# Kernel tuning notes

Hardware: AMD Instinct MI355X
Metric: run time of the kernel (lower is better)

## Reference

```python
import jax, jax.numpy as jnp
import numpy as np

T, B, E, H = 512, 32, 512, 2048

def setup_inputs() -> dict:
    key = jax.random.key(0)
    k1, k2, k3 = jax.random.split(key, 3)
    sent = jax.random.normal(k1, (T, B, E), dtype=jnp.float32)
    lengths = jax.random.randint(k2, (B,), 1, T + 1)  # unused by the math (pack is never applied)
    # Linear(E, 3H) params (PyTorch default-ish init scale)
    W = jax.random.normal(k3, (3 * H, E), dtype=jnp.float32) * (1.0 / np.sqrt(E))
    b = jnp.zeros((3 * H,), dtype=jnp.float32)
    return {"sent": sent, "lengths": lengths, "W": W, "b": b}

def reference(sent, lengths, W, b):
    # sent: (T, B, E) time-major. Single QRNN layer, window=1, output_gate=True, zoneout=0.
    Y = jnp.einsum('tbe,he->tbh', sent, W) + b          # (T, B, 3H)
    Z, F, O = jnp.split(Y, 3, axis=-1)
    Z = jnp.tanh(Z)
    F = jax.nn.sigmoid(F)
    O = jax.nn.sigmoid(O)

    # forget-mult recurrence: c_t = f_t * z_t + (1 - f_t) * c_{t-1}, c_0 = 0
    def step(c, zf):
        z, f = zf
        c = f * z + (1.0 - f) * c
        return c, c
    c0 = jnp.zeros_like(Z[0])                            # (B, H)
    _, C = jax.lax.scan(step, c0, (Z, F))                # (T, B, H)

    Hseq = O * C                                         # QRNN output (T, B, H)
    embeds = jnp.max(Hseq, axis=0)                       # torch.max(sent_output, 0)[0] -> (B, H)
    return embeds
```

## Files before the change

### kernel.cpp

```cpp
#include <hip/hip_runtime.h>
#include <stdint.h>

#define TT 512
#define BB 32
#define EE 512
#define HH 2048

typedef __attribute__((ext_vector_type(8))) short short8;
typedef __attribute__((ext_vector_type(4))) float f32x4;

#define XROW 528
#define XBUF (16 * XROW)

static __device__ __forceinline__ unsigned short f2bf(float f) {
    union { float f; unsigned u; } v; v.f = f;
    unsigned u = v.u;
    unsigned r = u + 0x7FFFu + ((u >> 16) & 1u);
    return (unsigned short)(r >> 16);
}

static __device__ __forceinline__ float fast_exp(float x) {
    return __builtin_amdgcn_exp2f(x * 1.44269504f);
}
static __device__ __forceinline__ float fast_rcp(float x) {
    return __builtin_amdgcn_rcpf(x);
}

static __device__ __forceinline__ void load_lds16(const unsigned short* g, unsigned short* l) {
    __builtin_amdgcn_global_load_lds(
        (const __attribute__((address_space(1))) unsigned int*)(uintptr_t)g,
        (__attribute__((address_space(3))) unsigned int*)(uintptr_t)l,
        16, 0, 0);
}

__global__ void convert_inputs(const float* __restrict__ X,
                               const float* __restrict__ W,
                               unsigned short* __restrict__ Xb,
                               unsigned short* __restrict__ Wb) {
    const int nX = TT * BB * EE;
    int i = (blockIdx.x * blockDim.x + threadIdx.x) * 8;
    const float* src;
    unsigned short* dst;
    int j;
    if (i < nX) { src = X; dst = Xb; j = i; }
    else        { src = W; dst = Wb; j = i - nX; }
    float4 v0 = *(const float4*)(src + j);
    float4 v1 = *(const float4*)(src + j + 4);
    union { short8 s; unsigned short u[8]; } o;
    o.u[0] = f2bf(v0.x); o.u[1] = f2bf(v0.y); o.u[2] = f2bf(v0.z); o.u[3] = f2bf(v0.w);
    o.u[4] = f2bf(v1.x); o.u[5] = f2bf(v1.y); o.u[6] = f2bf(v1.z); o.u[7] = f2bf(v1.w);
    *(short8*)(dst + j) = o.s;
}

__launch_bounds__(256, 2)
__global__ void qrnn_fused(const unsigned short* __restrict__ Xb,
                           const unsigned short* __restrict__ Wb,
                           const float* __restrict__ bias,
                           float* __restrict__ out)
{
    __shared__ unsigned short xlds[2 * XBUF];
    __shared__ float exch[2][2][64][12];

    const int tid  = threadIdx.x;
    const int wv   = tid >> 6;
    const int lane = tid & 63;
    const int q    = lane >> 4;
    const int c    = lane & 15;
    const int hi   = wv >> 1;
    const int s    = wv & 1;
    const int b    = blockIdx.y;
    const int h    = blockIdx.x * 32 + hi * 16 + c;

    short8 wz[8], wf[8], wo[8];
    {
        const unsigned short* wzr = Wb + (size_t)h * EE            + s * 256;
        const unsigned short* wfr = Wb + (size_t)(HH + h) * EE     + s * 256;
        const unsigned short* wor = Wb + (size_t)(2 * HH + h) * EE + s * 256;
#pragma unroll
        for (int k = 0; k < 8; ++k) {
            int e0 = k * 32 + q * 8;
            wz[k] = *(const short8*)(wzr + e0);
            wf[k] = *(const short8*)(wfr + e0);
            wo[k] = *(const short8*)(wor + e0);
        }
    }
#pragma unroll
    for (int k = 0; k < 8; ++k) {
        asm volatile("" : "+a"(wz[k]), "+a"(wf[k]), "+a"(wo[k]));
    }

    const float b0 = (s == 0) ? bias[h]          : 0.0f;
    const float b1 = (s == 0) ? bias[HH + h]     : 0.0f;
    const float b2 = (s == 0) ? bias[2 * HH + h] : 0.0f;

    float carry = 0.0f;
    float vmax  = -1e30f;

    const unsigned short* g0 = Xb + ((size_t)(wv * 4) * BB + b) * EE + lane * 8;
    unsigned short* l0 = &xlds[(wv * 4) * XROW];

    auto stage = [&](int n, int slot) {
        const unsigned short* g = g0 + (size_t)n * (16 * BB * EE);
        unsigned short* l = l0 + slot * XBUF;
#pragma unroll
        for (int i = 0; i < 4; ++i)
            load_lds16(g + (size_t)i * (BB * EE), l + i * XROW);
    };

    stage(0, 0);
    __syncthreads();

    for (int ch = 0; ch < 32; ++ch) {
        const int buf = ch & 1;
        if (ch < 31) stage(ch + 1, buf ^ 1);

        const unsigned short* Abase = &xlds[buf * XBUF + c * XROW + s * 256 + q * 8];
        short8 a[8];
#pragma unroll
        for (int k = 0; k < 8; ++k)
            a[k] = *(const short8*)(Abase + k * 32);

        f32x4 az = {b0, b0, b0, b0};
        f32x4 af = {b1, b1, b1, b1};
        f32x4 ao = {b2, b2, b2, b2};
#pragma unroll
        for (int k = 0; k < 8; ++k) {
            az = __builtin_amdgcn_mfma_f32_16x16x32_bf16(a[k], wz[k], az, 0, 0, 0);
            af = __builtin_amdgcn_mfma_f32_16x16x32_bf16(a[k], wf[k], af, 0, 0, 0);
            ao = __builtin_amdgcn_mfma_f32_16x16x32_bf16(a[k], wo[k], ao, 0, 0, 0);
        }

        const int eb = ch & 1;
        if (s == 1) {
            float* e = &exch[eb][hi][lane][0];
            *(f32x4*)(e)     = az;
            *(f32x4*)(e + 4) = af;
            *(f32x4*)(e + 8) = ao;
        }

        __syncthreads();

        if (s == 0) {
            const float* e = &exch[eb][hi][lane][0];
            f32x4 pz = *(const f32x4*)(e);
            f32x4 pf = *(const f32x4*)(e + 4);
            f32x4 po = *(const f32x4*)(e + 8);
            az = az + pz; af = af + pf; ao = ao + po;

            float aa[4], mm[4], oo[4];
#pragma unroll
            for (int r = 0; r < 4; ++r) {
                float e2 = fast_exp(2.0f * az[r]);
                float z  = 1.0f - 2.0f * fast_rcp(e2 + 1.0f);
                float f  = fast_rcp(1.0f + fast_exp(-af[r]));
                float o  = fast_rcp(1.0f + fast_exp(-ao[r]));
                aa[r] = f * z;
                mm[r] = 1.0f - f;
                oo[r] = o;
            }

            float A = aa[0], M = mm[0];
#pragma unroll
            for (int r = 1; r < 4; ++r) { A = aa[r] + mm[r] * A; M = mm[r] * M; }

            float Ap = __shfl_up(A, 16, 64), Mp = __shfl_up(M, 16, 64);
            if (q >= 1) { A = A + M * Ap; M = M * Mp; }
            Ap = __shfl_up(A, 32, 64); Mp = __shfl_up(M, 32, 64);
            if (q >= 2) { A = A + M * Ap; M = M * Mp; }
            float Ae = __shfl_up(A, 16, 64), Me = __shfl_up(M, 16, 64);
            if (q == 0) { Ae = 0.0f; Me = 1.0f; }
            float cc = Ae + Me * carry;

#pragma unroll
            for (int r = 0; r < 4; ++r) {
                cc = aa[r] + mm[r] * cc;
                vmax = fmaxf(vmax, oo[r] * cc);
            }

            float cend = A + M * carry;
            carry = __shfl(cend, 48 + c, 64);
        }
    }

    if (s == 0) {
        vmax = fmaxf(vmax, __shfl_xor(vmax, 16, 64));
        vmax = fmaxf(vmax, __shfl_xor(vmax, 32, 64));
        if (q == 0) out[(size_t)b * HH + h] = vmax;
    }
}

extern "C" void kernel_launch(void* const* d_in, const int* in_sizes, int n_in,
                              void* d_out, int out_size, void* d_ws, size_t ws_size,
                              hipStream_t stream) {
    const float* sent = (const float*)d_in[0];
    const float* W    = (const float*)d_in[2];
    const float* bias = (const float*)d_in[3];
    float* out        = (float*)d_out;

    const int nX = TT * BB * EE;
    const int nW = 3 * HH * EE;
    unsigned short* Xb = (unsigned short*)d_ws;
    unsigned short* Wb = Xb + nX;

    int totalVec = (nX + nW) / 8;
    convert_inputs<<<totalVec / 256, 256, 0, stream>>>(sent, W, Xb, Wb);

    dim3 grid(HH / 32, BB);
    qrnn_fused<<<grid, 256, 0, stream>>>(Xb, Wb, bias, out);
}
```

Before: 215.5 us.

## Software-pipeline the scan one chunk behind the MFMA and convert W in-kernel

The fused kernel now runs the nonlinearity and scan for chunk ch-1 while the MFMAs for chunk ch are issued, so the serial scan overlaps with tensor-core work and there is one barrier per iteration. The weights are now read as fp32 and converted to bf16 inside the fused kernel, so the separate conversion of W to a workspace is dropped. The in-kernel conversion uses scalar fp32 loads and each W row is re-converted by all 32 batch blocks, so it adds redundant global reads at kernel start. The pipelining also keeps extra accumulator registers live across iterations.

```diff
diff --git a/kernel.cpp b/kernel.cpp
--- a/kernel.cpp
+++ b/kernel.cpp
@@ -34,27 +34,19 @@
 }
 
 __global__ void convert_inputs(const float* __restrict__ X,
-                               const float* __restrict__ W,
-                               unsigned short* __restrict__ Xb,
-                               unsigned short* __restrict__ Wb) {
-    const int nX = TT * BB * EE;
+                               unsigned short* __restrict__ Xb) {
     int i = (blockIdx.x * blockDim.x + threadIdx.x) * 8;
-    const float* src;
-    unsigned short* dst;
-    int j;
-    if (i < nX) { src = X; dst = Xb; j = i; }
-    else        { src = W; dst = Wb; j = i - nX; }
-    float4 v0 = *(const float4*)(src + j);
-    float4 v1 = *(const float4*)(src + j + 4);
+    float4 v0 = *(const float4*)(X + i);
+    float4 v1 = *(const float4*)(X + i + 4);
     union { short8 s; unsigned short u[8]; } o;
     o.u[0] = f2bf(v0.x); o.u[1] = f2bf(v0.y); o.u[2] = f2bf(v0.z); o.u[3] = f2bf(v0.w);
     o.u[4] = f2bf(v1.x); o.u[5] = f2bf(v1.y); o.u[6] = f2bf(v1.z); o.u[7] = f2bf(v1.w);
-    *(short8*)(dst + j) = o.s;
+    *(short8*)(Xb + i) = o.s;
 }
 
 __launch_bounds__(256, 2)
 __global__ void qrnn_fused(const unsigned short* __restrict__ Xb,
-                           const unsigned short* __restrict__ Wb,
+                           const float* __restrict__ Wf,
                            const float* __restrict__ bias,
                            float* __restrict__ out)
 {
@@ -73,15 +65,20 @@
 
     short8 wz[8], wf[8], wo[8];
     {
-        const unsigned short* wzr = Wb + (size_t)h * EE            + s * 256;
-        const unsigned short* wfr = Wb + (size_t)(HH + h) * EE     + s * 256;
-        const unsigned short* wor = Wb + (size_t)(2 * HH + h) * EE + s * 256;
+        const float* wzr = Wf + (size_t)h * EE            + s * 256;
+        const float* wfr = Wf + (size_t)(HH + h) * EE     + s * 256;
+        const float* wor = Wf + (size_t)(2 * HH + h) * EE + s * 256;
 #pragma unroll
         for (int k = 0; k < 8; ++k) {
             int e0 = k * 32 + q * 8;
-            wz[k] = *(const short8*)(wzr + e0);
-            wf[k] = *(const short8*)(wfr + e0);
-            wo[k] = *(const short8*)(wor + e0);
+            union { short8 s8; unsigned short u[8]; } pz, pf, po;
+#pragma unroll
+            for (int j = 0; j < 8; ++j) {
+                pz.u[j] = f2bf(wzr[e0 + j]);
+                pf.u[j] = f2bf(wfr[e0 + j]);
+                po.u[j] = f2bf(wor[e0 + j]);
+            }
+            wz[k] = pz.s8; wf[k] = pf.s8; wo[k] = po.s8;
         }
     }
 #pragma unroll
@@ -110,50 +107,46 @@
     stage(0, 0);
     __syncthreads();
 
-    for (int ch = 0; ch < 32; ++ch) {
+    f32x4 yz = {0,0,0,0}, yf = {0,0,0,0}, yo = {0,0,0,0};
+
+    for (int ch = 0; ch <= 32; ++ch) {
         const int buf = ch & 1;
         if (ch < 31) stage(ch + 1, buf ^ 1);
 
-        const unsigned short* Abase = &xlds[buf * XBUF + c * XROW + s * 256 + q * 8];
-        short8 a[8];
-#pragma unroll
-        for (int k = 0; k < 8; ++k)
-            a[k] = *(const short8*)(Abase + k * 32);
-
-        f32x4 az = {b0, b0, b0, b0};
-        f32x4 af = {b1, b1, b1, b1};
-        f32x4 ao = {b2, b2, b2, b2};
-#pragma unroll
-        for (int k = 0; k < 8; ++k) {
-            az = __builtin_amdgcn_mfma_f32_16x16x32_bf16(a[k], wz[k], az, 0, 0, 0);
-            af = __builtin_amdgcn_mfma_f32_16x16x32_bf16(a[k], wf[k], af, 0, 0, 0);
-            ao = __builtin_amdgcn_mfma_f32_16x16x32_bf16(a[k], wo[k], ao, 0, 0, 0);
-        }
-
-        const int eb = ch & 1;
-        if (s == 1) {
-            float* e = &exch[eb][hi][lane][0];
-            *(f32x4*)(e)     = az;
-            *(f32x4*)(e + 4) = af;
-            *(f32x4*)(e + 8) = ao;
-        }
-
-        __syncthreads();
-
-        if (s == 0) {
+        f32x4 az, af, ao;
+        if (ch < 32) {
+            const unsigned short* Abase = &xlds[buf * XBUF + c * XROW + s * 256 + q * 8];
+            short8 a[8];
+#pragma unroll
+            for (int k = 0; k < 8; ++k)
+                a[k] = *(const short8*)(Abase + k * 32);
+
+            az = (f32x4){b0, b0, b0, b0};
+            af = (f32x4){b1, b1, b1, b1};
+            ao = (f32x4){b2, b2, b2, b2};
+#pragma unroll
+            for (int k = 0; k < 8; ++k) {
+                az = __builtin_amdgcn_mfma_f32_16x16x32_bf16(a[k], wz[k], az, 0, 0, 0);
+                af = __builtin_amdgcn_mfma_f32_16x16x32_bf16(a[k], wf[k], af, 0, 0, 0);
+                ao = __builtin_amdgcn_mfma_f32_16x16x32_bf16(a[k], wo[k], ao, 0, 0, 0);
+            }
+        }
+
+        if (ch > 0 && s == 0) {
+            const int eb = (ch - 1) & 1;
             const float* e = &exch[eb][hi][lane][0];
             f32x4 pz = *(const f32x4*)(e);
             f32x4 pf = *(const f32x4*)(e + 4);
             f32x4 po = *(const f32x4*)(e + 8);
-            az = az + pz; af = af + pf; ao = ao + po;
+            f32x4 tz = yz + pz, tf = yf + pf, to = yo + po;
 
             float aa[4], mm[4], oo[4];
 #pragma unroll
             for (int r = 0; r < 4; ++r) {
-                float e2 = fast_exp(2.0f * az[r]);
+                float e2 = fast_exp(2.0f * tz[r]);
                 float z  = 1.0f - 2.0f * fast_rcp(e2 + 1.0f);
-                float f  = fast_rcp(1.0f + fast_exp(-af[r]));
-                float o  = fast_rcp(1.0f + fast_exp(-ao[r]));
+                float f  = fast_rcp(1.0f + fast_exp(-tf[r]));
+                float o  = fast_rcp(1.0f + fast_exp(-to[r]));
                 aa[r] = f * z;
                 mm[r] = 1.0f - f;
                 oo[r] = o;
@@ -180,6 +173,17 @@
             float cend = A + M * carry;
             carry = __shfl(cend, 48 + c, 64);
         }
+
+        if (ch < 32 && s == 1) {
+            float* e = &exch[buf][hi][lane][0];
+            *(f32x4*)(e)     = az;
+            *(f32x4*)(e + 4) = af;
+            *(f32x4*)(e + 8) = ao;
+        }
+
+        if (ch < 32) __syncthreads();
+
+        if (ch < 32 && s == 0) { yz = az; yf = af; yo = ao; }
     }
 
     if (s == 0) {
@@ -198,13 +202,10 @@
     float* out        = (float*)d_out;
 
     const int nX = TT * BB * EE;
-    const int nW = 3 * HH * EE;
     unsigned short* Xb = (unsigned short*)d_ws;
-    unsigned short* Wb = Xb + nX;
-
-    int totalVec = (nX + nW) / 8;
-    convert_inputs<<<totalVec / 256, 256, 0, stream>>>(sent, W, Xb, Wb);
+
+    convert_inputs<<<nX / 8 / 256, 256, 0, stream>>>(sent, Xb);
 
     dim3 grid(HH / 32, BB);
-    qrnn_fused<<<grid, 256, 0, stream>>>(Xb, Wb, bias, out);
-}
+    qrnn_fused<<<grid, 256, 0, stream>>>(Xb, W, bias, out);
+}
```

New measurement: 252.8 us. 1.17x slower.

## Process 32 timesteps per chunk with single-buffered LDS and interleaved MFMA streams

Applied to the files above, without the earlier changes.

Doubles the timestep chunk from 16 to 32 and drops the LDS double buffer. Operands are loaded into registers first, then a barrier lets the next chunk's global-to-LDS staging overlap the MFMAs. The two 16-step sub-tiles run as interleaved independent MFMA chains and a two-segment scan, which halves the chunk iterations and barriers. The cost is more registers and an extra barrier per chunk, and with one buffer a chunk's prefetch can no longer start until every wave has finished reading the previous one.

```diff
diff --git a/kernel.cpp b/kernel.cpp
--- a/kernel.cpp
+++ b/kernel.cpp
@@ -10,7 +10,7 @@
 typedef __attribute__((ext_vector_type(4))) float f32x4;
 
 #define XROW 528
-#define XBUF (16 * XROW)
+#define XBUF (32 * XROW)
 
 static __device__ __forceinline__ unsigned short f2bf(float f) {
     union { float f; unsigned u; } v; v.f = f;
@@ -18,14 +18,12 @@
     unsigned r = u + 0x7FFFu + ((u >> 16) & 1u);
     return (unsigned short)(r >> 16);
 }
-
 static __device__ __forceinline__ float fast_exp(float x) {
     return __builtin_amdgcn_exp2f(x * 1.44269504f);
 }
 static __device__ __forceinline__ float fast_rcp(float x) {
     return __builtin_amdgcn_rcpf(x);
 }
-
 static __device__ __forceinline__ void load_lds16(const unsigned short* g, unsigned short* l) {
     __builtin_amdgcn_global_load_lds(
         (const __attribute__((address_space(1))) unsigned int*)(uintptr_t)g,
@@ -58,8 +56,8 @@
                            const float* __restrict__ bias,
                            float* __restrict__ out)
 {
-    __shared__ unsigned short xlds[2 * XBUF];
-    __shared__ float exch[2][2][64][12];
+    __shared__ unsigned short xlds[XBUF];
+    __shared__ float exch[2][64][28];
 
     const int tid  = threadIdx.x;
     const int wv   = tid >> 6;
@@ -96,89 +94,109 @@
     float carry = 0.0f;
     float vmax  = -1e30f;
 
-    const unsigned short* g0 = Xb + ((size_t)(wv * 4) * BB + b) * EE + lane * 8;
-    unsigned short* l0 = &xlds[(wv * 4) * XROW];
-
-    auto stage = [&](int n, int slot) {
-        const unsigned short* g = g0 + (size_t)n * (16 * BB * EE);
-        unsigned short* l = l0 + slot * XBUF;
-#pragma unroll
-        for (int i = 0; i < 4; ++i)
-            load_lds16(g + (size_t)i * (BB * EE), l + i * XROW);
+    const unsigned short* g0 = Xb + ((size_t)(wv * 8) * BB + b) * EE + lane * 8;
+    unsigned short* l0 = &xlds[(wv * 8) * XROW];
+    auto stage = [&](int n) {
+        const unsigned short* g = g0 + (size_t)n * (32 * BB * EE);
+#pragma unroll
+        for (int i = 0; i < 8; ++i)
+            load_lds16(g + (size_t)i * (BB * EE), l0 + i * XROW);
     };
 
-    stage(0, 0);
+    stage(0);
     __syncthreads();
 
-    for (int ch = 0; ch < 32; ++ch) {
-        const int buf = ch & 1;
-        if (ch < 31) stage(ch + 1, buf ^ 1);
-
-        const unsigned short* Abase = &xlds[buf * XBUF + c * XROW + s * 256 + q * 8];
-        short8 a[8];
-#pragma unroll
-        for (int k = 0; k < 8; ++k)
-            a[k] = *(const short8*)(Abase + k * 32);
-
-        f32x4 az = {b0, b0, b0, b0};
-        f32x4 af = {b1, b1, b1, b1};
-        f32x4 ao = {b2, b2, b2, b2};
+#pragma unroll 1
+    for (int ch = 0; ch < 16; ++ch) {
+        const unsigned short* Ab = &xlds[c * XROW + s * 256 + q * 8];
+        short8 a0[8], a1[8];
 #pragma unroll
         for (int k = 0; k < 8; ++k) {
-            az = __builtin_amdgcn_mfma_f32_16x16x32_bf16(a[k], wz[k], az, 0, 0, 0);
-            af = __builtin_amdgcn_mfma_f32_16x16x32_bf16(a[k], wf[k], af, 0, 0, 0);
-            ao = __builtin_amdgcn_mfma_f32_16x16x32_bf16(a[k], wo[k], ao, 0, 0, 0);
-        }
-
-        const int eb = ch & 1;
+            a0[k] = *(const short8*)(Ab + k * 32);
+            a1[k] = *(const short8*)(Ab + 16 * XROW + k * 32);
+        }
+
+        __syncthreads();
+
+        if (ch < 15) stage(ch + 1);
+
+        f32x4 az0 = {b0,b0,b0,b0}, af0 = {b1,b1,b1,b1}, ao0 = {b2,b2,b2,b2};
+        f32x4 az1 = {b0,b0,b0,b0}, af1 = {b1,b1,b1,b1}, ao1 = {b2,b2,b2,b2};
+#pragma unroll
+        for (int k = 0; k < 8; ++k) {
+            az0 = __builtin_amdgcn_mfma_f32_16x16x32_bf16(a0[k], wz[k], az0, 0, 0, 0);
+            az1 = __builtin_amdgcn_mfma_f32_16x16x32_bf16(a1[k], wz[k], az1, 0, 0, 0);
+            af0 = __builtin_amdgcn_mfma_f32_16x16x32_bf16(a0[k], wf[k], af0, 0, 0, 0);
+            af1 = __builtin_amdgcn_mfma_f32_16x16x32_bf16(a1[k], wf[k], af1, 0, 0, 0);
+            ao0 = __builtin_amdgcn_mfma_f32_16x16x32_bf16(a0[k], wo[k], ao0, 0, 0, 0);
+            ao1 = __builtin_amdgcn_mfma_f32_16x16x32_bf16(a1[k], wo[k], ao1, 0, 0, 0);
+        }
+
         if (s == 1) {
-            float* e = &exch[eb][hi][lane][0];
-            *(f32x4*)(e)     = az;
-            *(f32x4*)(e + 4) = af;
-            *(f32x4*)(e + 8) = ao;
+            float* e = &exch[hi][lane][0];
+            *(f32x4*)(e +  0) = az0;  *(f32x4*)(e +  4) = af0;  *(f32x4*)(e +  8) = ao0;
+            *(f32x4*)(e + 12) = az1;  *(f32x4*)(e + 16) = af1;  *(f32x4*)(e + 20) = ao1;
         }
 
         __syncthreads();
 
         if (s == 0) {
-            const float* e = &exch[eb][hi][lane][0];
-            f32x4 pz = *(const f32x4*)(e);
-            f32x4 pf = *(const f32x4*)(e + 4);
-            f32x4 po = *(const f32x4*)(e + 8);
-            az = az + pz; af = af + pf; ao = ao + po;
-
-            float aa[4], mm[4], oo[4];
+            const float* e = &exch[hi][lane][0];
+            f32x4 tz0 = az0 + *(const f32x4*)(e +  0);
+            f32x4 tf0 = af0 + *(const f32x4*)(e +  4);
+            f32x4 to0 = ao0 + *(const f32x4*)(e +  8);
+            f32x4 tz1 = az1 + *(const f32x4*)(e + 12);
+            f32x4 tf1 = af1 + *(const f32x4*)(e + 16);
+            f32x4 to1 = ao1 + *(const f32x4*)(e + 20);
+
+            float aa[2][4], mm[2][4], oo[2][4];
 #pragma unroll
             for (int r = 0; r < 4; ++r) {
-                float e2 = fast_exp(2.0f * az[r]);
+                float e2 = fast_exp(2.0f * tz0[r]);
                 float z  = 1.0f - 2.0f * fast_rcp(e2 + 1.0f);
-                float f  = fast_rcp(1.0f + fast_exp(-af[r]));
-                float o  = fast_rcp(1.0f + fast_exp(-ao[r]));
-                aa[r] = f * z;
-                mm[r] = 1.0f - f;
-                oo[r] = o;
-            }
-
-            float A = aa[0], M = mm[0];
-#pragma unroll
-            for (int r = 1; r < 4; ++r) { A = aa[r] + mm[r] * A; M = mm[r] * M; }
-
-            float Ap = __shfl_up(A, 16, 64), Mp = __shfl_up(M, 16, 64);
-            if (q >= 1) { A = A + M * Ap; M = M * Mp; }
-            Ap = __shfl_up(A, 32, 64); Mp = __shfl_up(M, 32, 64);
-            if (q >= 2) { A = A + M * Ap; M = M * Mp; }
-            float Ae = __shfl_up(A, 16, 64), Me = __shfl_up(M, 16, 64);
-            if (q == 0) { Ae = 0.0f; Me = 1.0f; }
-            float cc = Ae + Me * carry;
-
+                float f  = fast_rcp(1.0f + fast_exp(-tf0[r]));
+                oo[0][r] = fast_rcp(1.0f + fast_exp(-to0[r]));
+                aa[0][r] = f * z;  mm[0][r] = 1.0f - f;
+                float e2b = fast_exp(2.0f * tz1[r]);
+                float zb  = 1.0f - 2.0f * fast_rcp(e2b + 1.0f);
+                float fb  = fast_rcp(1.0f + fast_exp(-tf1[r]));
+                oo[1][r] = fast_rcp(1.0f + fast_exp(-to1[r]));
+                aa[1][r] = fb * zb;  mm[1][r] = 1.0f - fb;
+            }
+
+            float A0 = aa[0][0], M0 = mm[0][0], A1 = aa[1][0], M1 = mm[1][0];
+#pragma unroll
+            for (int r = 1; r < 4; ++r) {
+                A0 = aa[0][r] + mm[0][r] * A0;  M0 = mm[0][r] * M0;
+                A1 = aa[1][r] + mm[1][r] * A1;  M1 = mm[1][r] * M1;
+            }
+            float Ap, Mp, Bp, Np;
+            Ap = __shfl_up(A0, 16, 64); Mp = __shfl_up(M0, 16, 64);
+            Bp = __shfl_up(A1, 16, 64); Np = __shfl_up(M1, 16, 64);
+            if (q >= 1) { A0 = A0 + M0 * Ap; M0 *= Mp; A1 = A1 + M1 * Bp; M1 *= Np; }
+            Ap = __shfl_up(A0, 32, 64); Mp = __shfl_up(M0, 32, 64);
+            Bp = __shfl_up(A1, 32, 64); Np = __shfl_up(M1, 32, 64);
+            if (q >= 2) { A0 = A0 + M0 * Ap; M0 *= Mp; A1 = A1 + M1 * Bp; M1 *= Np; }
+            float fA0 = __shfl(A0, 48 + c, 64), fM0 = __shfl(M0, 48 + c, 64);
+            float fA1 = __shfl(A1, 48 + c, 64), fM1 = __shfl(M1, 48 + c, 64);
+            float eA0 = __shfl_up(A0, 16, 64), eM0 = __shfl_up(M0, 16, 64);
+            float eA1 = __shfl_up(A1, 16, 64), eM1 = __shfl_up(M1, 16, 64);
+            if (q == 0) { eA0 = 0.0f; eM0 = 1.0f; eA1 = 0.0f; eM1 = 1.0f; }
+
+            float cc = eA0 + eM0 * carry;
 #pragma unroll
             for (int r = 0; r < 4; ++r) {
-                cc = aa[r] + mm[r] * cc;
-                vmax = fmaxf(vmax, oo[r] * cc);
-            }
-
-            float cend = A + M * carry;
-            carry = __shfl(cend, 48 + c, 64);
+                cc = aa[0][r] + mm[0][r] * cc;
+                vmax = fmaxf(vmax, oo[0][r] * cc);
+            }
+            float base1 = fA0 + fM0 * carry;
+            cc = eA1 + eM1 * base1;
+#pragma unroll
+            for (int r = 0; r < 4; ++r) {
+                cc = aa[1][r] + mm[1][r] * cc;
+                vmax = fmaxf(vmax, oo[1][r] * cc);
+            }
+            carry = fA1 + fM1 * base1;
         }
     }
 
```

After: 231.0 us. 1.07x slower.

## Split GEMM and scan into dedicated warps with a one-chunk software pipeline

Applied to the files above, without the earlier changes.

The block grows from 4 to 6 waves. Four waves only run the MFMA GEMM and write partial sums to a double-buffered LDS exchange. Two extra waves add the partials, apply bias and the activations, and run the forget-mult scan one chunk behind. This is meant to overlap the serial scan and transcendental work with the next chunk's matrix multiply instead of running them back to back. In exchange it adds an extra loop iteration, more LDS traffic for the exchange, and more threads per block, which may reduce occupancy under launch bounds of 384 threads with 2 blocks per unit.

```diff
diff --git a/kernel.cpp b/kernel.cpp
--- a/kernel.cpp
+++ b/kernel.cpp
@@ -18,14 +18,12 @@
     unsigned r = u + 0x7FFFu + ((u >> 16) & 1u);
     return (unsigned short)(r >> 16);
 }
-
 static __device__ __forceinline__ float fast_exp(float x) {
     return __builtin_amdgcn_exp2f(x * 1.44269504f);
 }
 static __device__ __forceinline__ float fast_rcp(float x) {
     return __builtin_amdgcn_rcpf(x);
 }
-
 static __device__ __forceinline__ void load_lds16(const unsigned short* g, unsigned short* l) {
     __builtin_amdgcn_global_load_lds(
         (const __attribute__((address_space(1))) unsigned int*)(uintptr_t)g,
@@ -52,27 +50,29 @@
     *(short8*)(dst + j) = o.s;
 }
 
-__launch_bounds__(256, 2)
+__launch_bounds__(384, 2)
 __global__ void qrnn_fused(const unsigned short* __restrict__ Xb,
                            const unsigned short* __restrict__ Wb,
                            const float* __restrict__ bias,
                            float* __restrict__ out)
 {
     __shared__ unsigned short xlds[2 * XBUF];
-    __shared__ float exch[2][2][64][12];
+    __shared__ float exch[2][2][2][64][12];
 
     const int tid  = threadIdx.x;
     const int wv   = tid >> 6;
     const int lane = tid & 63;
     const int q    = lane >> 4;
     const int c    = lane & 15;
-    const int hi   = wv >> 1;
+    const int b    = blockIdx.y;
+    const bool isGemm = (wv < 4);
+    const int hi   = (wv >> 1) & 1;
     const int s    = wv & 1;
-    const int b    = blockIdx.y;
-    const int h    = blockIdx.x * 32 + hi * 16 + c;
+    const int shi  = wv - 4;
 
     short8 wz[8], wf[8], wo[8];
-    {
+    if (isGemm) {
+        const int h = blockIdx.x * 32 + hi * 16 + c;
         const unsigned short* wzr = Wb + (size_t)h * EE            + s * 256;
         const unsigned short* wfr = Wb + (size_t)(HH + h) * EE     + s * 256;
         const unsigned short* wor = Wb + (size_t)(2 * HH + h) * EE + s * 256;
@@ -83,22 +83,25 @@
             wf[k] = *(const short8*)(wfr + e0);
             wo[k] = *(const short8*)(wor + e0);
         }
-    }
-#pragma unroll
-    for (int k = 0; k < 8; ++k) {
-        asm volatile("" : "+a"(wz[k]), "+a"(wf[k]), "+a"(wo[k]));
-    }
-
-    const float b0 = (s == 0) ? bias[h]          : 0.0f;
-    const float b1 = (s == 0) ? bias[HH + h]     : 0.0f;
-    const float b2 = (s == 0) ? bias[2 * HH + h] : 0.0f;
+#pragma unroll
+        for (int k = 0; k < 8; ++k) {
+            asm volatile("" : "+a"(wz[k]), "+a"(wf[k]), "+a"(wo[k]));
+        }
+    }
+
+    float bz = 0.f, bfg = 0.f, bog = 0.f;
+    if (!isGemm) {
+        const int h = blockIdx.x * 32 + shi * 16 + c;
+        bz  = bias[h];
+        bfg = bias[HH + h];
+        bog = bias[2 * HH + h];
+    }
 
     float carry = 0.0f;
     float vmax  = -1e30f;
 
-    const unsigned short* g0 = Xb + ((size_t)(wv * 4) * BB + b) * EE + lane * 8;
-    unsigned short* l0 = &xlds[(wv * 4) * XROW];
-
+    const unsigned short* g0 = Xb + ((size_t)((wv & 3) * 4) * BB + b) * EE + lane * 8;
+    unsigned short* l0 = &xlds[((wv & 3) * 4) * XROW];
     auto stage = [&](int n, int slot) {
         const unsigned short* g = g0 + (size_t)n * (16 * BB * EE);
         unsigned short* l = l0 + slot * XBUF;
@@ -107,53 +110,53 @@
             load_lds16(g + (size_t)i * (BB * EE), l + i * XROW);
     };
 
-    stage(0, 0);
+    if (isGemm) stage(0, 0);
     __syncthreads();
 
-    for (int ch = 0; ch < 32; ++ch) {
-        const int buf = ch & 1;
-        if (ch < 31) stage(ch + 1, buf ^ 1);
-
-        const unsigned short* Abase = &xlds[buf * XBUF + c * XROW + s * 256 + q * 8];
-        short8 a[8];
-#pragma unroll
-        for (int k = 0; k < 8; ++k)
-            a[k] = *(const short8*)(Abase + k * 32);
-
-        f32x4 az = {b0, b0, b0, b0};
-        f32x4 af = {b1, b1, b1, b1};
-        f32x4 ao = {b2, b2, b2, b2};
-#pragma unroll
-        for (int k = 0; k < 8; ++k) {
-            az = __builtin_amdgcn_mfma_f32_16x16x32_bf16(a[k], wz[k], az, 0, 0, 0);
-            af = __builtin_amdgcn_mfma_f32_16x16x32_bf16(a[k], wf[k], af, 0, 0, 0);
-            ao = __builtin_amdgcn_mfma_f32_16x16x32_bf16(a[k], wo[k], ao, 0, 0, 0);
-        }
-
-        const int eb = ch & 1;
-        if (s == 1) {
-            float* e = &exch[eb][hi][lane][0];
-            *(f32x4*)(e)     = az;
-            *(f32x4*)(e + 4) = af;
-            *(f32x4*)(e + 8) = ao;
-        }
-
-        __syncthreads();
-
-        if (s == 0) {
-            const float* e = &exch[eb][hi][lane][0];
-            f32x4 pz = *(const f32x4*)(e);
-            f32x4 pf = *(const f32x4*)(e + 4);
-            f32x4 po = *(const f32x4*)(e + 8);
-            az = az + pz; af = af + pf; ao = ao + po;
+#pragma unroll 1
+    for (int ch = 0; ch <= 32; ++ch) {
+        if (isGemm) {
+            if (ch < 32) {
+                const int buf = ch & 1;
+                if (ch < 31) stage(ch + 1, buf ^ 1);
+
+                const unsigned short* Ab = &xlds[buf * XBUF + c * XROW + s * 256 + q * 8];
+                short8 a[8];
+#pragma unroll
+                for (int k = 0; k < 8; ++k)
+                    a[k] = *(const short8*)(Ab + k * 32);
+
+                f32x4 az = {0.f,0.f,0.f,0.f}, af = {0.f,0.f,0.f,0.f}, ao = {0.f,0.f,0.f,0.f};
+#pragma unroll
+                for (int k = 0; k < 8; ++k) {
+                    az = __builtin_amdgcn_mfma_f32_16x16x32_bf16(a[k], wz[k], az, 0, 0, 0);
+                    af = __builtin_amdgcn_mfma_f32_16x16x32_bf16(a[k], wf[k], af, 0, 0, 0);
+                    ao = __builtin_amdgcn_mfma_f32_16x16x32_bf16(a[k], wo[k], ao, 0, 0, 0);
+                }
+
+                float* e = &exch[buf][hi][s][lane][0];
+                *(f32x4*)(e)     = az;
+                *(f32x4*)(e + 4) = af;
+                *(f32x4*)(e + 8) = ao;
+            }
+        } else if (ch > 0) {
+            const int slot = (ch - 1) & 1;
+            const float* e0 = &exch[slot][shi][0][lane][0];
+            const float* e1 = &exch[slot][shi][1][lane][0];
+            f32x4 tz = *(const f32x4*)(e0)     + *(const f32x4*)(e1);
+            f32x4 tf = *(const f32x4*)(e0 + 4) + *(const f32x4*)(e1 + 4);
+            f32x4 to = *(const f32x4*)(e0 + 8) + *(const f32x4*)(e1 + 8);
 
             float aa[4], mm[4], oo[4];
 #pragma unroll
             for (int r = 0; r < 4; ++r) {
-                float e2 = fast_exp(2.0f * az[r]);
+                float yz = tz[r] + bz;
+                float yf = tf[r] + bfg;
+                float yo = to[r] + bog;
+                float e2 = fast_exp(2.0f * yz);
                 float z  = 1.0f - 2.0f * fast_rcp(e2 + 1.0f);
-                float f  = fast_rcp(1.0f + fast_exp(-af[r]));
-                float o  = fast_rcp(1.0f + fast_exp(-ao[r]));
+                float f  = fast_rcp(1.0f + fast_exp(-yf));
+                float o  = fast_rcp(1.0f + fast_exp(-yo));
                 aa[r] = f * z;
                 mm[r] = 1.0f - f;
                 oo[r] = o;
@@ -180,12 +183,17 @@
             float cend = A + M * carry;
             carry = __shfl(cend, 48 + c, 64);
         }
-    }
-
-    if (s == 0) {
+
+        __syncthreads();
+    }
+
+    if (!isGemm) {
         vmax = fmaxf(vmax, __shfl_xor(vmax, 16, 64));
         vmax = fmaxf(vmax, __shfl_xor(vmax, 32, 64));
-        if (q == 0) out[(size_t)b * HH + h] = vmax;
+        if (q == 0) {
+            const int h = blockIdx.x * 32 + shi * 16 + c;
+            out[(size_t)b * HH + h] = vmax;
+        }
     }
 }
 
@@ -206,5 +214,5 @@
     convert_inputs<<<totalVec / 256, 256, 0, stream>>>(sent, W, Xb, Wb);
 
     dim3 grid(HH / 32, BB);
-    qrnn_fused<<<grid, 256, 0, stream>>>(Xb, Wb, bias, out);
-}
+    qrnn_fused<<<grid, 384, 0, stream>>>(Xb, Wb, bias, out);
+}
```

After: 284.4 us. +32.0%, slower.
